# Kernel tuning notes

Measured on AMD Instinct MI355X. Metric: run time of the kernel, lower is better.

The kernel has to match this reference:

```python
import jax, jax.numpy as jnp
import numpy as np
from jax import lax

B, T = 64, 2048
D_ENC, D_RNN, D_ATT = 512, 1024, 128
NF, K = 32, 31


def setup_inputs() -> dict:
    key = jax.random.key(0)
    ks = jax.random.split(key, 9)
    return {
        "attention_hidden_state": jax.random.normal(ks[0], (B, D_RNN), jnp.float32),
        "memory": jax.random.normal(ks[1], (B, T, D_ENC), jnp.float32),
        "processed_memory": jax.random.normal(ks[2], (B, T, D_ATT), jnp.float32),
        "attention_weights_cat": jax.random.uniform(ks[3], (B, 2, T), jnp.float32),
        "mask": jnp.zeros((B, T), dtype=bool),
        "query_w": jax.random.normal(ks[4], (D_ATT, D_RNN), jnp.float32) * 0.02,
        "value_w": jax.random.normal(ks[5], (1, D_ATT), jnp.float32) * 0.05,
        "loc_conv_w": jax.random.normal(ks[6], (NF, 2, K), jnp.float32) * 0.1,
        "loc_dense_w": jax.random.normal(ks[7], (D_ATT, NF), jnp.float32) * 0.1,
    }


def reference(attention_hidden_state, memory, processed_memory,
              attention_weights_cat, mask, query_w, value_w,
              loc_conv_w, loc_dense_w):
    k = loc_conv_w.shape[-1]
    pad = (k - 1) // 2
    # processed query: [B, 1, D_ATT]
    pq = (attention_hidden_state @ query_w.T)[:, None, :]
    # location features: Conv1d(2->NF, 'same' pad, no bias) then dense NF->D_ATT
    loc = lax.conv_general_dilated(
        attention_weights_cat, loc_conv_w,
        window_strides=(1,), padding=[(pad, pad)],
        dimension_numbers=("NCH", "OIH", "NCH"))  # [B, NF, T]
    loc = jnp.einsum("bft,af->bta", loc, loc_dense_w)  # [B, T, D_ATT]
    # additive energies
    energies = jnp.tanh(pq + processed_memory + loc)  # [B, T, D_ATT]
    alignment = jnp.einsum("bta,a->bt", energies, value_w[0])  # [B, T]
    alignment = jnp.where(mask, -jnp.inf, alignment)
    attention_weights = jax.nn.softmax(alignment, axis=1)  # [B, T]
    attention_context = jnp.einsum("bt,btd->bd", attention_weights, memory)
    return attention_context, attention_weights
```

## Files before the change

kernel.cpp:

```cpp
#include <hip/hip_runtime.h>
#include <hip/hip_bf16.h>

#define BB 64
#define TT 2048
#define D_ENC 512
#define D_RNN 1024
#define D_ATT 128
#define NF 32
#define KW 31

__global__ __launch_bounds__(256) void pq_kernel(
    const float* __restrict__ hid, const float* __restrict__ qw,
    float* __restrict__ pq)
{
    int b = blockIdx.x;
    int wave = threadIdx.x >> 6, lane = threadIdx.x & 63;
    int a = blockIdx.y * 4 + wave;
    const float* hrow = hid + (size_t)b * D_RNN;
    const float* qrow = qw + (size_t)a * D_RNN;
    float acc = 0.f;
#pragma unroll
    for (int j = 0; j < 4; ++j) {
        int k = (j * 64 + lane) * 4;
        float4 h = *(const float4*)(hrow + k);
        float4 q = *(const float4*)(qrow + k);
        acc += h.x * q.x + h.y * q.y + h.z * q.z + h.w * q.w;
    }
#pragma unroll
    for (int off = 32; off; off >>= 1) acc += __shfl_xor(acc, off, 64);
    if (lane == 0) pq[b * D_ATT + a] = acc;
}

__global__ __launch_bounds__(256) void fused_kernel(
    const float* __restrict__ pm,
    const float* __restrict__ awcat,
    const unsigned char* __restrict__ mask,
    const float* __restrict__ convw,
    const float* __restrict__ ldw,
    const float* __restrict__ vw,
    const float* __restrict__ pq,
    const float* __restrict__ mem,
    float* __restrict__ wts,
    float* __restrict__ ctx,
    float* __restrict__ sums)
{
    __shared__ float s_aw[2 * 160];
    __shared__ float s_loc[128 * NF];
    __shared__ float s_e[128];
    __shared__ float4 s_p[128];

    int b = blockIdx.x;
    int t0 = blockIdx.y * 128;
    int tid = threadIdx.x;

    for (int i = tid; i < 320; i += 256) {
        int c = i / 160, j = i % 160;
        int tg = t0 - 15 + j;
        float v = 0.f;
        if (tg >= 0 && tg < TT) v = awcat[((size_t)b * 2 + c) * TT + tg];
        s_aw[c * 160 + j] = v;
    }
    __syncthreads();

    {
        int f = tid & 31, g = tid >> 5;
        float w[2 * KW];
#pragma unroll
        for (int j = 0; j < 2 * KW; ++j) w[j] = convw[f * 2 * KW + j];
#pragma unroll
        for (int p = 0; p < 4; ++p) {
            int tb = g * 16 + p * 4;
            float a0 = 0.f, a1 = 0.f, a2 = 0.f, a3 = 0.f;
#pragma unroll
            for (int c = 0; c < 2; ++c) {
                float x[34];
#pragma unroll
                for (int j = 0; j < 34; ++j) x[j] = s_aw[c * 160 + tb + j];
#pragma unroll
                for (int k = 0; k < KW; ++k) {
                    float wk = w[c * KW + k];
                    a0 += x[k] * wk; a1 += x[k + 1] * wk;
                    a2 += x[k + 2] * wk; a3 += x[k + 3] * wk;
                }
            }
            s_loc[(tb + 0) * NF + f] = a0;
            s_loc[(tb + 1) * NF + f] = a1;
            s_loc[(tb + 2) * NF + f] = a2;
            s_loc[(tb + 3) * NF + f] = a3;
        }
    }
    __syncthreads();

    {
        int wave = tid >> 6, lane = tid & 63;
        float pq0 = pq[b * 128 + lane], pq1 = pq[b * 128 + 64 + lane];
        float vw0 = vw[lane], vw1 = vw[64 + lane];
        float4 lA[8], lB[8];
#pragma unroll
        for (int f4 = 0; f4 < 8; ++f4) {
            lA[f4] = *(const float4*)(ldw + lane * NF + f4 * 4);
            lB[f4] = *(const float4*)(ldw + (64 + lane) * NF + f4 * 4);
        }
        const float* pmb = pm + ((size_t)b * TT + t0) * 128;
        for (int i = 0; i < 32; ++i) {
            int t = wave * 32 + i;
            float pm0 = pmb[(size_t)t * 128 + lane];
            float pm1 = pmb[(size_t)t * 128 + 64 + lane];
            float dA = 0.f, dB = 0.f;
#pragma unroll
            for (int f4 = 0; f4 < 8; ++f4) {
                float4 lv = *(const float4*)&s_loc[t * NF + f4 * 4];
                dA += lv.x * lA[f4].x + lv.y * lA[f4].y + lv.z * lA[f4].z + lv.w * lA[f4].w;
                dB += lv.x * lB[f4].x + lv.y * lB[f4].y + lv.z * lB[f4].z + lv.w * lB[f4].w;
            }
            float xA = pq0 + pm0 + dA, xB = pq1 + pm1 + dB;
            float eA = 1.0f - __fdividef(2.0f, __expf(2.0f * xA) + 1.0f);
            float eB = 1.0f - __fdividef(2.0f, __expf(2.0f * xB) + 1.0f);
            float al = vw0 * eA + vw1 * eB;
#pragma unroll
            for (int off = 32; off; off >>= 1) al += __shfl_xor(al, off, 64);
            if (lane == 0) {
                int tt = t0 + t;
                bool m = mask[(size_t)b * TT + tt] != 0;
                float e = m ? 0.f : __expf(al);
                s_e[t] = e;
                wts[(size_t)b * TT + tt] = e;
            }
        }
    }
    __syncthreads();

    if (tid < 64) {
        float s = s_e[tid] + s_e[tid + 64];
#pragma unroll
        for (int off = 32; off; off >>= 1) s += __shfl_xor(s, off, 64);
        if (tid == 0) atomicAdd(&sums[b], s);
    }

    {
        int d4 = tid & 127;
        int th = tid >> 7;
        const float4* mrow = (const float4*)(mem + ((size_t)b * TT + t0) * D_ENC);
        float4 acc = {0.f, 0.f, 0.f, 0.f};
        for (int i = th; i < 128; i += 2) {
            float w = s_e[i];
            float4 m = mrow[(size_t)i * 128 + d4];
            acc.x += w * m.x; acc.y += w * m.y; acc.z += w * m.z; acc.w += w * m.w;
        }
        if (th == 1) s_p[d4] = acc;
        __syncthreads();
        if (th == 0) {
            float4 o = s_p[d4];
            float* dst = ctx + (size_t)b * D_ENC + d4 * 4;
            atomicAdd(dst + 0, acc.x + o.x);
            atomicAdd(dst + 1, acc.y + o.y);
            atomicAdd(dst + 2, acc.z + o.z);
            atomicAdd(dst + 3, acc.w + o.w);
        }
    }
}

__global__ __launch_bounds__(256) void finalize_kernel(
    float* __restrict__ wts, float* __restrict__ ctx,
    const float* __restrict__ sums)
{
    int b = blockIdx.x, tid = threadIdx.x;
    float inv = __fdividef(1.0f, sums[b]);
    float* wrow = wts + (size_t)b * TT;
#pragma unroll
    for (int i = 0; i < 8; ++i) wrow[tid + i * 256] *= inv;
    float* crow = ctx + (size_t)b * D_ENC;
    crow[tid] *= inv;
    crow[tid + 256] *= inv;
}

extern "C" void kernel_launch(void* const* d_in, const int* in_sizes, int n_in,
                              void* d_out, int out_size, void* d_ws, size_t ws_size,
                              hipStream_t stream)
{
    const float* hid  = (const float*)d_in[0];
    const float* mem  = (const float*)d_in[1];
    const float* pm   = (const float*)d_in[2];
    const float* aw   = (const float*)d_in[3];
    const unsigned char* mask = (const unsigned char*)d_in[4];
    const float* qw   = (const float*)d_in[5];
    const float* vw   = (const float*)d_in[6];
    const float* cw   = (const float*)d_in[7];
    const float* ldw  = (const float*)d_in[8];

    float* out = (float*)d_out;
    float* ctx = out;
    float* wts = out + BB * D_ENC;
    float* pq  = (float*)d_ws;
    float* sums = pq + BB * D_ATT;

    hipMemsetAsync(ctx, 0, (size_t)BB * D_ENC * sizeof(float), stream);
    hipMemsetAsync(sums, 0, (size_t)BB * sizeof(float), stream);
    pq_kernel<<<dim3(BB, 32), 256, 0, stream>>>(hid, qw, pq);
    fused_kernel<<<dim3(BB, TT / 128), 256, 0, stream>>>(
        pm, aw, mask, cw, ldw, vw, pq, mem, wts, ctx, sums);
    finalize_kernel<<<BB, 256, 0, stream>>>(wts, ctx, sums);
}
```

Measured before the change: 503.8 us.

## Split fused attention kernel into alignment and context kernels, stage conv weights in LDS

```diff
diff --git a/kernel.cpp b/kernel.cpp
--- a/kernel.cpp
+++ b/kernel.cpp
@@ -31,7 +31,7 @@
     if (lane == 0) pq[b * D_ATT + a] = acc;
 }
 
-__global__ __launch_bounds__(256) void fused_kernel(
+__global__ __launch_bounds__(256, 2) void align_kernel(
     const float* __restrict__ pm,
     const float* __restrict__ awcat,
     const unsigned char* __restrict__ mask,
@@ -39,15 +39,13 @@
     const float* __restrict__ ldw,
     const float* __restrict__ vw,
     const float* __restrict__ pq,
-    const float* __restrict__ mem,
     float* __restrict__ wts,
-    float* __restrict__ ctx,
     float* __restrict__ sums)
 {
     __shared__ float s_aw[2 * 160];
+    __shared__ float s_cw[NF * 63];
     __shared__ float s_loc[128 * NF];
     __shared__ float s_e[128];
-    __shared__ float4 s_p[128];
 
     int b = blockIdx.x;
     int t0 = blockIdx.y * 128;
@@ -60,13 +58,15 @@
         if (tg >= 0 && tg < TT) v = awcat[((size_t)b * 2 + c) * TT + tg];
         s_aw[c * 160 + j] = v;
     }
+    for (int i = tid; i < NF * 62; i += 256) {
+        int f = i / 62, j = i - f * 62;
+        s_cw[f * 63 + j] = convw[i];
+    }
     __syncthreads();
 
     {
         int f = tid & 31, g = tid >> 5;
-        float w[2 * KW];
-#pragma unroll
-        for (int j = 0; j < 2 * KW; ++j) w[j] = convw[f * 2 * KW + j];
+        int wbase = f * 63;
 #pragma unroll
         for (int p = 0; p < 4; ++p) {
             int tb = g * 16 + p * 4;
@@ -78,7 +78,7 @@
                 for (int j = 0; j < 34; ++j) x[j] = s_aw[c * 160 + tb + j];
 #pragma unroll
                 for (int k = 0; k < KW; ++k) {
-                    float wk = w[c * KW + k];
+                    float wk = s_cw[wbase + c * 31 + k];
                     a0 += x[k] * wk; a1 += x[k + 1] * wk;
                     a2 += x[k + 2] * wk; a3 += x[k + 3] * wk;
                 }
@@ -93,19 +93,19 @@
 
     {
         int wave = tid >> 6, lane = tid & 63;
-        float pq0 = pq[b * 128 + lane], pq1 = pq[b * 128 + 64 + lane];
-        float vw0 = vw[lane], vw1 = vw[64 + lane];
+        float2 pq2 = *(const float2*)(pq + b * 128 + 2 * lane);
+        float2 vw2 = *(const float2*)(vw + 2 * lane);
         float4 lA[8], lB[8];
 #pragma unroll
         for (int f4 = 0; f4 < 8; ++f4) {
-            lA[f4] = *(const float4*)(ldw + lane * NF + f4 * 4);
-            lB[f4] = *(const float4*)(ldw + (64 + lane) * NF + f4 * 4);
+            lA[f4] = *(const float4*)(ldw + (2 * lane) * NF + f4 * 4);
+            lB[f4] = *(const float4*)(ldw + (2 * lane + 1) * NF + f4 * 4);
         }
         const float* pmb = pm + ((size_t)b * TT + t0) * 128;
+#pragma unroll 4
         for (int i = 0; i < 32; ++i) {
             int t = wave * 32 + i;
-            float pm0 = pmb[(size_t)t * 128 + lane];
-            float pm1 = pmb[(size_t)t * 128 + 64 + lane];
+            float2 pmv = *(const float2*)(pmb + (size_t)t * 128 + 2 * lane);
             float dA = 0.f, dB = 0.f;
 #pragma unroll
             for (int f4 = 0; f4 < 8; ++f4) {
@@ -113,10 +113,10 @@
                 dA += lv.x * lA[f4].x + lv.y * lA[f4].y + lv.z * lA[f4].z + lv.w * lA[f4].w;
                 dB += lv.x * lB[f4].x + lv.y * lB[f4].y + lv.z * lB[f4].z + lv.w * lB[f4].w;
             }
-            float xA = pq0 + pm0 + dA, xB = pq1 + pm1 + dB;
+            float xA = pq2.x + pmv.x + dA, xB = pq2.y + pmv.y + dB;
             float eA = 1.0f - __fdividef(2.0f, __expf(2.0f * xA) + 1.0f);
             float eB = 1.0f - __fdividef(2.0f, __expf(2.0f * xB) + 1.0f);
-            float al = vw0 * eA + vw1 * eB;
+            float al = vw2.x * eA + vw2.y * eB;
 #pragma unroll
             for (int off = 32; off; off >>= 1) al += __shfl_xor(al, off, 64);
             if (lane == 0) {
@@ -136,27 +136,39 @@
         for (int off = 32; off; off >>= 1) s += __shfl_xor(s, off, 64);
         if (tid == 0) atomicAdd(&sums[b], s);
     }
-
-    {
-        int d4 = tid & 127;
-        int th = tid >> 7;
-        const float4* mrow = (const float4*)(mem + ((size_t)b * TT + t0) * D_ENC);
-        float4 acc = {0.f, 0.f, 0.f, 0.f};
-        for (int i = th; i < 128; i += 2) {
-            float w = s_e[i];
-            float4 m = mrow[(size_t)i * 128 + d4];
-            acc.x += w * m.x; acc.y += w * m.y; acc.z += w * m.z; acc.w += w * m.w;
-        }
-        if (th == 1) s_p[d4] = acc;
-        __syncthreads();
-        if (th == 0) {
-            float4 o = s_p[d4];
-            float* dst = ctx + (size_t)b * D_ENC + d4 * 4;
-            atomicAdd(dst + 0, acc.x + o.x);
-            atomicAdd(dst + 1, acc.y + o.y);
-            atomicAdd(dst + 2, acc.z + o.z);
-            atomicAdd(dst + 3, acc.w + o.w);
-        }
+}
+
+__global__ __launch_bounds__(256) void ctx_kernel(
+    const float* __restrict__ mem, const float* __restrict__ wts,
+    float* __restrict__ out)
+{
+    int b = blockIdx.x, c = blockIdx.y;
+    int tid = threadIdx.x;
+    int d4 = tid & 127;
+    int th = tid >> 7;
+    int t0 = c * 64;
+    __shared__ float s_w[64];
+    __shared__ float4 s_p[128];
+    if (tid < 64) s_w[tid] = wts[(size_t)b * TT + t0 + tid];
+    __syncthreads();
+    const float4* mrow = (const float4*)(mem + ((size_t)b * TT + t0) * D_ENC);
+    float4 acc = {0.f, 0.f, 0.f, 0.f};
+#pragma unroll 8
+    for (int ii = 0; ii < 32; ++ii) {
+        int i = ii * 2 + th;
+        float w = s_w[i];
+        float4 m = mrow[(size_t)i * 128 + d4];
+        acc.x += w * m.x; acc.y += w * m.y; acc.z += w * m.z; acc.w += w * m.w;
+    }
+    if (th == 1) s_p[d4] = acc;
+    __syncthreads();
+    if (th == 0) {
+        float4 o = s_p[d4];
+        float* dst = out + (size_t)b * D_ENC + d4 * 4;
+        atomicAdd(dst + 0, acc.x + o.x);
+        atomicAdd(dst + 1, acc.y + o.y);
+        atomicAdd(dst + 2, acc.z + o.z);
+        atomicAdd(dst + 3, acc.w + o.w);
     }
 }
 
@@ -197,7 +209,8 @@
     hipMemsetAsync(ctx, 0, (size_t)BB * D_ENC * sizeof(float), stream);
     hipMemsetAsync(sums, 0, (size_t)BB * sizeof(float), stream);
     pq_kernel<<<dim3(BB, 32), 256, 0, stream>>>(hid, qw, pq);
-    fused_kernel<<<dim3(BB, TT / 128), 256, 0, stream>>>(
-        pm, aw, mask, cw, ldw, vw, pq, mem, wts, ctx, sums);
+    align_kernel<<<dim3(BB, TT / 128), 256, 0, stream>>>(
+        pm, aw, mask, cw, ldw, vw, pq, wts, sums);
+    ctx_kernel<<<dim3(BB, 32), 256, 0, stream>>>(mem, wts, ctx);
     finalize_kernel<<<BB, 256, 0, stream>>>(wts, ctx, sums);
 }
```

New measurement: 500.1 us. No clear change (-0.7%).
